# Performance work log

Measured on AMD Instinct MI355X. Metric: run time of the kernel, lower is better.

Reference implementation:

```python
import jax, jax.numpy as jnp
import numpy as np

N_NODES = 100000
N_EDGES = 3200000
N_GRAPHS = 5000
IN_DIM = 11 + 3  # QM9 num_features + pos
HID = 64


def setup_inputs() -> dict:
    key = jax.random.key(0)
    ks = jax.random.split(key, 12)
    x = jax.random.normal(ks[0], (N_NODES, 11), dtype=jnp.float32)
    pos = jax.random.normal(ks[1], (N_NODES, 3), dtype=jnp.float32)
    edge_index = jax.random.randint(ks[2], (2, N_EDGES), 0, N_NODES, dtype=jnp.int32)
    batch = jnp.sort(jax.random.randint(ks[3], (N_NODES,), 0, N_GRAPHS, dtype=jnp.int32))
    s1 = 1.0 / np.sqrt(IN_DIM)
    s2 = 1.0 / np.sqrt(HID)
    return {
        'x': x,
        'pos': pos,
        'edge_index': edge_index,
        'batch': batch,
        'W1_l': jax.random.uniform(ks[4], (IN_DIM, HID), jnp.float32, -s1, s1),
        'W1_r': jax.random.uniform(ks[5], (IN_DIM, HID), jnp.float32, -s1, s1),
        'b1': jax.random.uniform(ks[6], (HID,), jnp.float32, -s1, s1),
        'W2_l': jax.random.uniform(ks[7], (HID, HID), jnp.float32, -s2, s2),
        'W2_r': jax.random.uniform(ks[8], (HID, HID), jnp.float32, -s2, s2),
        'b2': jax.random.uniform(ks[9], (HID,), jnp.float32, -s2, s2),
        'W_lin': jax.random.uniform(ks[10], (HID, 1), jnp.float32, -s2, s2),
        'b_lin': jax.random.uniform(ks[11], (1,), jnp.float32, -s2, s2),
    }


def _sage_conv(h, src, dst, W_l, W_r, b):
    # mean-aggregate source features at target nodes (PyG SAGEConv default)
    msg = h[src]  # [E, D] gather
    agg = jax.ops.segment_sum(msg, dst, num_segments=N_NODES)
    deg = jax.ops.segment_sum(jnp.ones((src.shape[0],), h.dtype), dst, num_segments=N_NODES)
    agg = agg / jnp.maximum(deg, 1.0)[:, None]
    return agg @ W_l + h @ W_r + b


def reference(x, pos, edge_index, batch, W1_l, W1_r, b1, W2_l, W2_r, b2, W_lin, b_lin):
    h = jnp.concatenate([x, pos], axis=1)  # [N, 14]
    src, dst = edge_index[0], edge_index[1]
    h = jax.nn.relu(_sage_conv(h, src, dst, W1_l, W1_r, b1))
    h = jax.nn.relu(_sage_conv(h, src, dst, W2_l, W2_r, b2))
    # global mean pool over graphs
    pooled = jax.ops.segment_sum(h, batch, num_segments=N_GRAPHS)
    cnt = jax.ops.segment_sum(jnp.ones((N_NODES,), h.dtype), batch, num_segments=N_GRAPHS)
    pooled = pooled / jnp.maximum(cnt, 1.0)[:, None]
    return pooled @ W_lin + b_lin  # [G, 1]
```

## Files before the change

### kernel.cpp

```cpp
#include <hip/hip_runtime.h>

#define IND 14
#define INDP 16
#define HIDD 64
#define RB 512
#define NB_MAX 256
#define BH_BLOCKS 512

__global__ void build_h0p(const float* __restrict__ x, const float* __restrict__ pos,
                          float* __restrict__ h0p, int N) {
    int tid = blockIdx.x * blockDim.x + threadIdx.x;
    int total = N * INDP;
    if (tid >= total) return;
    int n = tid >> 4, d = tid & 15;
    float v = 0.0f;
    if (d < 11) v = x[n * 11 + d];
    else if (d < 14) v = pos[n * 3 + (d - 11)];
    h0p[tid] = v;
}

__global__ __launch_bounds__(256) void bhist(const int* __restrict__ ei,
                                             int* __restrict__ gcount,
                                             int E, int NB, int chunk) {
    __shared__ int cntS[NB_MAX];
    cntS[threadIdx.x] = 0;
    if (threadIdx.x + 128 < NB_MAX) {}
    __syncthreads();
    int start = blockIdx.x * chunk;
    int end = min(start + chunk, E);
    for (int e = start + threadIdx.x; e < end; e += 256)
        atomicAdd(&cntS[ei[E + e] >> 9], 1);
    __syncthreads();
    if (threadIdx.x < NB)
        gcount[(size_t)threadIdx.x * BH_BLOCKS + blockIdx.x] = cntS[threadIdx.x];
}

__global__ __launch_bounds__(256) void bscan1(const int* __restrict__ gcount,
                                              int* __restrict__ gbase,
                                              int* __restrict__ btot, int NB) {
    int wave = blockIdx.x * 4 + (threadIdx.x >> 6);
    int lane = threadIdx.x & 63;
    if (wave >= NB) return;
    const int* src = gcount + (size_t)wave * BH_BLOCKS;
    int* dstp = gbase + (size_t)wave * BH_BLOCKS;
    int run = 0;
#pragma unroll
    for (int r = 0; r < 8; ++r) {
        int val = src[r * 64 + lane];
        int inc = val;
#pragma unroll
        for (int off = 1; off < 64; off <<= 1) {
            int tv = __shfl_up(inc, off, 64);
            if (lane >= off) inc += tv;
        }
        dstp[r * 64 + lane] = run + inc - val;
        run += __shfl(inc, 63, 64);
    }
    if (lane == 0) btot[wave] = run;
}

__global__ void bscan2(const int* __restrict__ btot, int* __restrict__ bbase,
                       int* __restrict__ rowptr, int NB, int N, int E) {
    int lane = threadIdx.x;
    int run = 0;
#pragma unroll
    for (int r = 0; r < 4; ++r) {
        int i = r * 64 + lane;
        int val = (i < NB) ? btot[i] : 0;
        int inc = val;
#pragma unroll
        for (int off = 1; off < 64; off <<= 1) {
            int tv = __shfl_up(inc, off, 64);
            if (lane >= off) inc += tv;
        }
        if (i < NB) bbase[i] = run + inc - val;
        run += __shfl(inc, 63, 64);
    }
    if (lane == 0) rowptr[N] = E;
}

__global__ __launch_bounds__(256) void bscatter(const int* __restrict__ ei,
                                                const int* __restrict__ gbase,
                                                const int* __restrict__ bbase,
                                                int2* __restrict__ pairs,
                                                int E, int NB, int chunk) {
    __shared__ int cur[NB_MAX];
    if (threadIdx.x < NB)
        cur[threadIdx.x] = bbase[threadIdx.x] +
                           gbase[(size_t)threadIdx.x * BH_BLOCKS + blockIdx.x];
    __syncthreads();
    int start = blockIdx.x * chunk;
    int end = min(start + chunk, E);
    for (int e = start + threadIdx.x; e < end; e += 256) {
        int s = ei[e], d = ei[E + e];
        int p = atomicAdd(&cur[d >> 9], 1);
        pairs[p] = make_int2(s, d);
    }
}

__global__ __launch_bounds__(1024) void csr_build(const int2* __restrict__ pairs,
                                                  const int* __restrict__ btot,
                                                  const int* __restrict__ bbase,
                                                  int* __restrict__ rowptr,
                                                  int* __restrict__ csr, int N) {
    __shared__ int s[RB];
    __shared__ int fillS[RB];
    int b = blockIdx.x;
    int cnt = btot[b], base = bbase[b];
    int t = threadIdx.x;
    if (t < RB) { s[t] = 0; fillS[t] = 0; }
    __syncthreads();
    for (int i = t; i < cnt; i += 1024)
        atomicAdd(&s[pairs[base + i].y & (RB - 1)], 1);
    __syncthreads();
    for (int off = 1; off < RB; off <<= 1) {
        int v = 0;
        if (t < RB && t >= off) v = s[t - off];
        __syncthreads();
        if (t < RB) s[t] += v;
        __syncthreads();
    }
    int node0 = b << 9;
    if (t < RB) {
        int node = node0 + t;
        if (node < N) rowptr[node] = base + (t ? s[t - 1] : 0);
    }
    __syncthreads();
    for (int i = t; i < cnt; i += 1024) {
        int2 pr = pairs[base + i];
        int local = pr.y & (RB - 1);
        int p = atomicAdd(&fillS[local], 1);
        int segbase = local ? s[local - 1] : 0;
        csr[base + segbase + p] = pr.x;
    }
}

__global__ __launch_bounds__(512) void agg_layer1(
        const float* __restrict__ h0p, const int* __restrict__ rowptr,
        const int* __restrict__ csr,
        const float* __restrict__ W_l, const float* __restrict__ W_r,
        const float* __restrict__ b, float* __restrict__ h1, int N) {
    __shared__ float sWl[IND * HIDD];
    __shared__ float sWr[IND * HIDD];
    __shared__ float sA[8][INDP];
    __shared__ float sS[8][INDP];
    for (int i = threadIdx.x; i < IND * HIDD; i += 512) {
        sWl[i] = W_l[i];
        sWr[i] = W_r[i];
    }
    int w = threadIdx.x >> 6, t = threadIdx.x & 63;
    int node = blockIdx.x * 8 + w;
    if (node < N) {
        int beg = rowptr[node], end = rowptr[node + 1];
        int s = t >> 2, q = t & 3;
        float4 acc = make_float4(0.f, 0.f, 0.f, 0.f);
        for (int e = beg + s; e < end; e += 16) {
            int idx = csr[e];
            const float4 v = *(const float4*)(h0p + (size_t)idx * INDP + q * 4);
            acc.x += v.x; acc.y += v.y; acc.z += v.z; acc.w += v.w;
        }
#pragma unroll
        for (int m = 4; m < 64; m <<= 1) {
            acc.x += __shfl_xor(acc.x, m, 64);
            acc.y += __shfl_xor(acc.y, m, 64);
            acc.z += __shfl_xor(acc.z, m, 64);
            acc.w += __shfl_xor(acc.w, m, 64);
        }
        float invd = 1.0f / fmaxf((float)(end - beg), 1.0f);
        if (t < 4)
            *(float4*)(&sA[w][t * 4]) =
                make_float4(acc.x * invd, acc.y * invd, acc.z * invd, acc.w * invd);
        if (t < INDP) sS[w][t] = h0p[(size_t)node * INDP + t];
    }
    __syncthreads();
    if (node >= N) return;
    float acc = b[t];
#pragma unroll
    for (int k = 0; k < IND; ++k)
        acc += sA[w][k] * sWl[k * HIDD + t] + sS[w][k] * sWr[k * HIDD + t];
    h1[(size_t)node * HIDD + t] = fmaxf(acc, 0.0f);
}

__global__ __launch_bounds__(512) void agg_layer2(
        const float* __restrict__ h1, const int* __restrict__ rowptr,
        const int* __restrict__ csr, const int* __restrict__ batch,
        const float* __restrict__ W_l, const float* __restrict__ W_r,
        const float* __restrict__ b,
        float* __restrict__ pooled, float* __restrict__ cnt, int N) {
    __shared__ float sWl[HIDD * HIDD];
    __shared__ float sWr[HIDD * HIDD];
    __shared__ float sA[8][HIDD];
    __shared__ float sS[8][HIDD];
    for (int i = threadIdx.x; i < HIDD * HIDD; i += 512) {
        sWl[i] = W_l[i];
        sWr[i] = W_r[i];
    }
    int w = threadIdx.x >> 6, t = threadIdx.x & 63;
    int node = blockIdx.x * 8 + w;
    if (node < N) {
        int beg = rowptr[node], end = rowptr[node + 1];
        int s = t >> 4, q = t & 15;
        float4 a0 = make_float4(0.f, 0.f, 0.f, 0.f);
        float4 a1 = make_float4(0.f, 0.f, 0.f, 0.f);
        int e = beg + s;
        for (; e + 4 < end; e += 8) {
            int i0 = csr[e];
            int i1 = csr[e + 4];
            const float4 v0 = *(const float4*)(h1 + (size_t)i0 * HIDD + q * 4);
            const float4 v1 = *(const float4*)(h1 + (size_t)i1 * HIDD + q * 4);
            a0.x += v0.x; a0.y += v0.y; a0.z += v0.z; a0.w += v0.w;
            a1.x += v1.x; a1.y += v1.y; a1.z += v1.z; a1.w += v1.w;
        }
        if (e < end) {
            int i0 = csr[e];
            const float4 v0 = *(const float4*)(h1 + (size_t)i0 * HIDD + q * 4);
            a0.x += v0.x; a0.y += v0.y; a0.z += v0.z; a0.w += v0.w;
        }
        a0.x += a1.x; a0.y += a1.y; a0.z += a1.z; a0.w += a1.w;
#pragma unroll
        for (int m = 16; m < 64; m <<= 1) {
            a0.x += __shfl_xor(a0.x, m, 64);
            a0.y += __shfl_xor(a0.y, m, 64);
            a0.z += __shfl_xor(a0.z, m, 64);
            a0.w += __shfl_xor(a0.w, m, 64);
        }
        float invd = 1.0f / fmaxf((float)(end - beg), 1.0f);
        if (t < 16)
            *(float4*)(&sA[w][t * 4]) =
                make_float4(a0.x * invd, a0.y * invd, a0.z * invd, a0.w * invd);
        sS[w][t] = h1[(size_t)node * HIDD + t];
    }
    __syncthreads();
    if (node >= N) return;
    float acc = b[t];
#pragma unroll 8
    for (int k = 0; k < HIDD; ++k)
        acc += sA[w][k] * sWl[k * HIDD + t] + sS[w][k] * sWr[k * HIDD + t];
    float val = fmaxf(acc, 0.0f);
    int g = batch[node];
    atomicAdd(pooled + (size_t)g * HIDD + t, val);
    if (t == 0) atomicAdd(cnt + g, 1.0f);
}

__global__ void final_k(const float* __restrict__ pooled, const float* __restrict__ cnt,
                        const float* __restrict__ W, const float* __restrict__ bl,
                        float* __restrict__ out, int G) {
    int g = blockIdx.x;
    if (g >= G) return;
    int t = threadIdx.x;
    float invc = 1.0f / fmaxf(cnt[g], 1.0f);
    float v = pooled[(size_t)g * HIDD + t] * invc * W[t];
#pragma unroll
    for (int o = 32; o > 0; o >>= 1) v += __shfl_down(v, o, 64);
    if (t == 0) out[g] = v + bl[0];
}

extern "C" void kernel_launch(void* const* d_in, const int* in_sizes, int n_in,
                              void* d_out, int out_size, void* d_ws, size_t ws_size,
                              hipStream_t stream) {
    const float* x   = (const float*)d_in[0];
    const float* pos = (const float*)d_in[1];
    const int* ei    = (const int*)d_in[2];
    const int* batch = (const int*)d_in[3];
    const float* W1l = (const float*)d_in[4];
    const float* W1r = (const float*)d_in[5];
    const float* b1  = (const float*)d_in[6];
    const float* W2l = (const float*)d_in[7];
    const float* W2r = (const float*)d_in[8];
    const float* b2  = (const float*)d_in[9];
    const float* Wl  = (const float*)d_in[10];
    const float* bl  = (const float*)d_in[11];
    float* out = (float*)d_out;

    int N = in_sizes[3];
    int E = in_sizes[2] / 2;
    int G = out_size;
    int NB = (N + RB - 1) >> 9;
    int chunk = (E + BH_BLOCKS - 1) / BH_BLOCKS;

    char* ws = (char*)d_ws;
    size_t off = 0;
    float* cnt = (float*)(ws + off);    off += (size_t)G * 4;
    float* pooled = (float*)(ws + off); off += (size_t)G * HIDD * 4;
    size_t zero_bytes = off;
    int* gcount = (int*)(ws + off);     off += (size_t)NB_MAX * BH_BLOCKS * 4;
    int* gbase  = (int*)(ws + off);     off += (size_t)NB_MAX * BH_BLOCKS * 4;
    int* btot   = (int*)(ws + off);     off += (size_t)NB_MAX * 4;
    int* bbase  = (int*)(ws + off);     off += (size_t)NB_MAX * 4;
    int* rowptr = (int*)(ws + off);     off += (size_t)(N + 1) * 4;
    off = (off + 255) & ~(size_t)255;
    int2* pairs = (int2*)(ws + off);    off += (size_t)E * 8;
    int* csr    = (int*)(ws + off);     off += (size_t)E * 4;
    off = (off + 255) & ~(size_t)255;
    float* h0p  = (float*)(ws + off);   off += (size_t)N * INDP * 4;
    off = (off + 255) & ~(size_t)255;
    float* h1   = (float*)(ws + off);   off += (size_t)N * HIDD * 4;

    hipMemsetAsync(d_ws, 0, zero_bytes, stream);

    int blk = 256;
    build_h0p<<<((size_t)N * INDP + blk - 1) / blk, blk, 0, stream>>>(x, pos, h0p, N);
    bhist<<<BH_BLOCKS, 256, 0, stream>>>(ei, gcount, E, NB, chunk);
    bscan1<<<(NB + 3) / 4, 256, 0, stream>>>(gcount, gbase, btot, NB);
    bscan2<<<1, 64, 0, stream>>>(btot, bbase, rowptr, NB, N, E);
    bscatter<<<BH_BLOCKS, 256, 0, stream>>>(ei, gbase, bbase, pairs, E, NB, chunk);
    csr_build<<<NB, 1024, 0, stream>>>(pairs, btot, bbase, rowptr, csr, N);
    agg_layer1<<<(N + 7) / 8, 512, 0, stream>>>(h0p, rowptr, csr, W1l, W1r, b1, h1, N);
    agg_layer2<<<(N + 7) / 8, 512, 0, stream>>>(h1, rowptr, csr, batch, W2l, W2r, b2,
                                                pooled, cnt, N);
    final_k<<<G, 64, 0, stream>>>(pooled, cnt, Wl, bl, out, G);
}
```

Baseline: 390.5 us.

## Gather neighbor features in bf16 and pack edge pairs into 32-bit words

Adds bf16 copies of the layer-0 and layer-1 node features and uses them for the neighbor gathers in both aggregation kernels, accumulating in fp32. The self term still reads the fp32 copy. This halves the bytes moved by the random per-edge gathers. Separately, the bucketed edge pairs are packed into one 32-bit word (local dst in the high bits, src in the low 17 bits), which halves the scatter and CSR-build traffic. The costs are bf16 rounding in the mean aggregation, extra writes for the dual-precision copies, and a src index limited to 17 bits.

```diff
diff --git a/kernel.cpp b/kernel.cpp
--- a/kernel.cpp
+++ b/kernel.cpp
@@ -7,8 +7,19 @@
 #define NB_MAX 256
 #define BH_BLOCKS 512
 
+typedef unsigned int uint;
+typedef unsigned short ushort;
+
+__device__ __forceinline__ float bf16lo(uint u) { return __uint_as_float(u << 16); }
+__device__ __forceinline__ float bf16hi(uint u) { return __uint_as_float(u & 0xFFFF0000u); }
+__device__ __forceinline__ ushort f2bf(float f) {
+    uint u = __float_as_uint(f);
+    u += 0x7FFFu + ((u >> 16) & 1u);
+    return (ushort)(u >> 16);
+}
+
 __global__ void build_h0p(const float* __restrict__ x, const float* __restrict__ pos,
-                          float* __restrict__ h0p, int N) {
+                          float* __restrict__ h0p, ushort* __restrict__ h0h, int N) {
     int tid = blockIdx.x * blockDim.x + threadIdx.x;
     int total = N * INDP;
     if (tid >= total) return;
@@ -17,6 +28,7 @@
     if (d < 11) v = x[n * 11 + d];
     else if (d < 14) v = pos[n * 3 + (d - 11)];
     h0p[tid] = v;
+    h0h[tid] = f2bf(v);
 }
 
 __global__ __launch_bounds__(256) void bhist(const int* __restrict__ ei,
@@ -24,7 +36,6 @@
                                              int E, int NB, int chunk) {
     __shared__ int cntS[NB_MAX];
     cntS[threadIdx.x] = 0;
-    if (threadIdx.x + 128 < NB_MAX) {}
     __syncthreads();
     int start = blockIdx.x * chunk;
     int end = min(start + chunk, E);
@@ -82,7 +93,7 @@
 __global__ __launch_bounds__(256) void bscatter(const int* __restrict__ ei,
                                                 const int* __restrict__ gbase,
                                                 const int* __restrict__ bbase,
-                                                int2* __restrict__ pairs,
+                                                uint* __restrict__ pairs,
                                                 int E, int NB, int chunk) {
     __shared__ int cur[NB_MAX];
     if (threadIdx.x < NB)
@@ -94,11 +105,11 @@
     for (int e = start + threadIdx.x; e < end; e += 256) {
         int s = ei[e], d = ei[E + e];
         int p = atomicAdd(&cur[d >> 9], 1);
-        pairs[p] = make_int2(s, d);
-    }
-}
-
-__global__ __launch_bounds__(1024) void csr_build(const int2* __restrict__ pairs,
+        pairs[p] = ((uint)(d & (RB - 1)) << 17) | (uint)s;
+    }
+}
+
+__global__ __launch_bounds__(1024) void csr_build(const uint* __restrict__ pairs,
                                                   const int* __restrict__ btot,
                                                   const int* __restrict__ bbase,
                                                   int* __restrict__ rowptr,
@@ -111,7 +122,7 @@
     if (t < RB) { s[t] = 0; fillS[t] = 0; }
     __syncthreads();
     for (int i = t; i < cnt; i += 1024)
-        atomicAdd(&s[pairs[base + i].y & (RB - 1)], 1);
+        atomicAdd(&s[pairs[base + i] >> 17], 1);
     __syncthreads();
     for (int off = 1; off < RB; off <<= 1) {
         int v = 0;
@@ -127,19 +138,20 @@
     }
     __syncthreads();
     for (int i = t; i < cnt; i += 1024) {
-        int2 pr = pairs[base + i];
-        int local = pr.y & (RB - 1);
+        uint pk = pairs[base + i];
+        int local = pk >> 17;
         int p = atomicAdd(&fillS[local], 1);
         int segbase = local ? s[local - 1] : 0;
-        csr[base + segbase + p] = pr.x;
+        csr[base + segbase + p] = (int)(pk & 0x1FFFFu);
     }
 }
 
 __global__ __launch_bounds__(512) void agg_layer1(
-        const float* __restrict__ h0p, const int* __restrict__ rowptr,
-        const int* __restrict__ csr,
+        const float* __restrict__ h0p, const ushort* __restrict__ h0h,
+        const int* __restrict__ rowptr, const int* __restrict__ csr,
         const float* __restrict__ W_l, const float* __restrict__ W_r,
-        const float* __restrict__ b, float* __restrict__ h1, int N) {
+        const float* __restrict__ b, float* __restrict__ h1f,
+        ushort* __restrict__ h1h, int N) {
     __shared__ float sWl[IND * HIDD];
     __shared__ float sWr[IND * HIDD];
     __shared__ float sA[8][INDP];
@@ -152,24 +164,26 @@
     int node = blockIdx.x * 8 + w;
     if (node < N) {
         int beg = rowptr[node], end = rowptr[node + 1];
-        int s = t >> 2, q = t & 3;
-        float4 acc = make_float4(0.f, 0.f, 0.f, 0.f);
-        for (int e = beg + s; e < end; e += 16) {
+        int s = t >> 1, hf = t & 1;
+        float acc[8] = {0.f, 0.f, 0.f, 0.f, 0.f, 0.f, 0.f, 0.f};
+        for (int e = beg + s; e < end; e += 32) {
             int idx = csr[e];
-            const float4 v = *(const float4*)(h0p + (size_t)idx * INDP + q * 4);
-            acc.x += v.x; acc.y += v.y; acc.z += v.z; acc.w += v.w;
-        }
-#pragma unroll
-        for (int m = 4; m < 64; m <<= 1) {
-            acc.x += __shfl_xor(acc.x, m, 64);
-            acc.y += __shfl_xor(acc.y, m, 64);
-            acc.z += __shfl_xor(acc.z, m, 64);
-            acc.w += __shfl_xor(acc.w, m, 64);
+            const uint4 v = *(const uint4*)(h0h + (size_t)idx * INDP + hf * 8);
+            acc[0] += bf16lo(v.x); acc[1] += bf16hi(v.x);
+            acc[2] += bf16lo(v.y); acc[3] += bf16hi(v.y);
+            acc[4] += bf16lo(v.z); acc[5] += bf16hi(v.z);
+            acc[6] += bf16lo(v.w); acc[7] += bf16hi(v.w);
+        }
+#pragma unroll
+        for (int m = 2; m < 64; m <<= 1) {
+#pragma unroll
+            for (int j = 0; j < 8; ++j) acc[j] += __shfl_xor(acc[j], m, 64);
         }
         float invd = 1.0f / fmaxf((float)(end - beg), 1.0f);
-        if (t < 4)
-            *(float4*)(&sA[w][t * 4]) =
-                make_float4(acc.x * invd, acc.y * invd, acc.z * invd, acc.w * invd);
+        if (t < 2) {
+#pragma unroll
+            for (int j = 0; j < 8; ++j) sA[w][t * 8 + j] = acc[j] * invd;
+        }
         if (t < INDP) sS[w][t] = h0p[(size_t)node * INDP + t];
     }
     __syncthreads();
@@ -178,12 +192,15 @@
 #pragma unroll
     for (int k = 0; k < IND; ++k)
         acc += sA[w][k] * sWl[k * HIDD + t] + sS[w][k] * sWr[k * HIDD + t];
-    h1[(size_t)node * HIDD + t] = fmaxf(acc, 0.0f);
+    float val = fmaxf(acc, 0.0f);
+    h1f[(size_t)node * HIDD + t] = val;
+    h1h[(size_t)node * HIDD + t] = f2bf(val);
 }
 
 __global__ __launch_bounds__(512) void agg_layer2(
-        const float* __restrict__ h1, const int* __restrict__ rowptr,
-        const int* __restrict__ csr, const int* __restrict__ batch,
+        const float* __restrict__ h1f, const ushort* __restrict__ h1h,
+        const int* __restrict__ rowptr, const int* __restrict__ csr,
+        const int* __restrict__ batch,
         const float* __restrict__ W_l, const float* __restrict__ W_r,
         const float* __restrict__ b,
         float* __restrict__ pooled, float* __restrict__ cnt, int N) {
@@ -199,36 +216,45 @@
     int node = blockIdx.x * 8 + w;
     if (node < N) {
         int beg = rowptr[node], end = rowptr[node + 1];
-        int s = t >> 4, q = t & 15;
-        float4 a0 = make_float4(0.f, 0.f, 0.f, 0.f);
-        float4 a1 = make_float4(0.f, 0.f, 0.f, 0.f);
+        int s = t >> 3, p = t & 7;
+        float a0[8] = {0.f, 0.f, 0.f, 0.f, 0.f, 0.f, 0.f, 0.f};
+        float a1[8] = {0.f, 0.f, 0.f, 0.f, 0.f, 0.f, 0.f, 0.f};
         int e = beg + s;
-        for (; e + 4 < end; e += 8) {
+        for (; e + 8 < end; e += 16) {
             int i0 = csr[e];
-            int i1 = csr[e + 4];
-            const float4 v0 = *(const float4*)(h1 + (size_t)i0 * HIDD + q * 4);
-            const float4 v1 = *(const float4*)(h1 + (size_t)i1 * HIDD + q * 4);
-            a0.x += v0.x; a0.y += v0.y; a0.z += v0.z; a0.w += v0.w;
-            a1.x += v1.x; a1.y += v1.y; a1.z += v1.z; a1.w += v1.w;
+            int i1 = csr[e + 8];
+            const uint4 v0 = *(const uint4*)(h1h + (size_t)i0 * HIDD + p * 8);
+            const uint4 v1 = *(const uint4*)(h1h + (size_t)i1 * HIDD + p * 8);
+            a0[0] += bf16lo(v0.x); a0[1] += bf16hi(v0.x);
+            a0[2] += bf16lo(v0.y); a0[3] += bf16hi(v0.y);
+            a0[4] += bf16lo(v0.z); a0[5] += bf16hi(v0.z);
+            a0[6] += bf16lo(v0.w); a0[7] += bf16hi(v0.w);
+            a1[0] += bf16lo(v1.x); a1[1] += bf16hi(v1.x);
+            a1[2] += bf16lo(v1.y); a1[3] += bf16hi(v1.y);
+            a1[4] += bf16lo(v1.z); a1[5] += bf16hi(v1.z);
+            a1[6] += bf16lo(v1.w); a1[7] += bf16hi(v1.w);
         }
         if (e < end) {
             int i0 = csr[e];
-            const float4 v0 = *(const float4*)(h1 + (size_t)i0 * HIDD + q * 4);
-            a0.x += v0.x; a0.y += v0.y; a0.z += v0.z; a0.w += v0.w;
-        }
-        a0.x += a1.x; a0.y += a1.y; a0.z += a1.z; a0.w += a1.w;
-#pragma unroll
-        for (int m = 16; m < 64; m <<= 1) {
-            a0.x += __shfl_xor(a0.x, m, 64);
-            a0.y += __shfl_xor(a0.y, m, 64);
-            a0.z += __shfl_xor(a0.z, m, 64);
-            a0.w += __shfl_xor(a0.w, m, 64);
+            const uint4 v0 = *(const uint4*)(h1h + (size_t)i0 * HIDD + p * 8);
+            a0[0] += bf16lo(v0.x); a0[1] += bf16hi(v0.x);
+            a0[2] += bf16lo(v0.y); a0[3] += bf16hi(v0.y);
+            a0[4] += bf16lo(v0.z); a0[5] += bf16hi(v0.z);
+            a0[6] += bf16lo(v0.w); a0[7] += bf16hi(v0.w);
+        }
+#pragma unroll
+        for (int j = 0; j < 8; ++j) a0[j] += a1[j];
+#pragma unroll
+        for (int m = 8; m < 64; m <<= 1) {
+#pragma unroll
+            for (int j = 0; j < 8; ++j) a0[j] += __shfl_xor(a0[j], m, 64);
         }
         float invd = 1.0f / fmaxf((float)(end - beg), 1.0f);
-        if (t < 16)
-            *(float4*)(&sA[w][t * 4]) =
-                make_float4(a0.x * invd, a0.y * invd, a0.z * invd, a0.w * invd);
-        sS[w][t] = h1[(size_t)node * HIDD + t];
+        if (t < 8) {
+#pragma unroll
+            for (int j = 0; j < 8; ++j) sA[w][t * 8 + j] = a0[j] * invd;
+        }
+        sS[w][t] = h1f[(size_t)node * HIDD + t];
     }
     __syncthreads();
     if (node >= N) return;
@@ -289,24 +315,29 @@
     int* bbase  = (int*)(ws + off);     off += (size_t)NB_MAX * 4;
     int* rowptr = (int*)(ws + off);     off += (size_t)(N + 1) * 4;
     off = (off + 255) & ~(size_t)255;
-    int2* pairs = (int2*)(ws + off);    off += (size_t)E * 8;
+    uint* pairs = (uint*)(ws + off);    off += (size_t)E * 4;
     int* csr    = (int*)(ws + off);     off += (size_t)E * 4;
     off = (off + 255) & ~(size_t)255;
     float* h0p  = (float*)(ws + off);   off += (size_t)N * INDP * 4;
     off = (off + 255) & ~(size_t)255;
-    float* h1   = (float*)(ws + off);   off += (size_t)N * HIDD * 4;
+    ushort* h0h = (ushort*)(ws + off);  off += (size_t)N * INDP * 2;
+    off = (off + 255) & ~(size_t)255;
+    float* h1f  = (float*)(ws + off);   off += (size_t)N * HIDD * 4;
+    off = (off + 255) & ~(size_t)255;
+    ushort* h1h = (ushort*)(ws + off);  off += (size_t)N * HIDD * 2;
 
     hipMemsetAsync(d_ws, 0, zero_bytes, stream);
 
     int blk = 256;
-    build_h0p<<<((size_t)N * INDP + blk - 1) / blk, blk, 0, stream>>>(x, pos, h0p, N);
+    build_h0p<<<((size_t)N * INDP + blk - 1) / blk, blk, 0, stream>>>(x, pos, h0p, h0h, N);
     bhist<<<BH_BLOCKS, 256, 0, stream>>>(ei, gcount, E, NB, chunk);
     bscan1<<<(NB + 3) / 4, 256, 0, stream>>>(gcount, gbase, btot, NB);
     bscan2<<<1, 64, 0, stream>>>(btot, bbase, rowptr, NB, N, E);
     bscatter<<<BH_BLOCKS, 256, 0, stream>>>(ei, gbase, bbase, pairs, E, NB, chunk);
     csr_build<<<NB, 1024, 0, stream>>>(pairs, btot, bbase, rowptr, csr, N);
-    agg_layer1<<<(N + 7) / 8, 512, 0, stream>>>(h0p, rowptr, csr, W1l, W1r, b1, h1, N);
-    agg_layer2<<<(N + 7) / 8, 512, 0, stream>>>(h1, rowptr, csr, batch, W2l, W2r, b2,
-                                                pooled, cnt, N);
+    agg_layer1<<<(N + 7) / 8, 512, 0, stream>>>(h0p, h0h, rowptr, csr, W1l, W1r, b1,
+                                                h1f, h1h, N);
+    agg_layer2<<<(N + 7) / 8, 512, 0, stream>>>(h1f, h1h, rowptr, csr, batch,
+                                                W2l, W2r, b2, pooled, cnt, N);
     final_k<<<G, 64, 0, stream>>>(pooled, cnt, Wl, bl, out, G);
 }
```

Result: faster. 370.6 us (-5.1%).
